# Kernel tuning notes

Hardware: AMD Instinct MI355X
Metric: run time of the kernel (lower is better)

## Reference

```python
import jax, jax.numpy as jnp
import numpy as np
import math

D_MODEL = 96
D_STATE = 16
D_CONV = 3
EXPAND = 2
D_INNER = EXPAND * D_MODEL          # 192
DT_RANK = math.ceil(D_MODEL / 16)   # 6
B_SZ, H_SZ, W_SZ = 2, 56, 56


def setup_inputs() -> dict:
    key = jax.random.key(0)
    ks = jax.random.split(key, 10)
    x = jax.random.normal(ks[0], (B_SZ, H_SZ, W_SZ, D_MODEL), jnp.float32)
    W_in = jax.random.normal(ks[1], (D_MODEL, 2 * D_INNER), jnp.float32) * 0.02
    conv_w = jax.random.normal(ks[2], (D_CONV, D_CONV, 1, D_INNER), jnp.float32) * 0.1
    conv_b = jax.random.normal(ks[3], (D_INNER,), jnp.float32) * 0.02
    W_xproj = jax.random.normal(ks[4], (D_INNER, DT_RANK + 2 * D_STATE), jnp.float32) * 0.02
    dt_std = DT_RANK ** -0.5
    W_dt = jax.random.uniform(ks[5], (DT_RANK, D_INNER), jnp.float32, -dt_std, dt_std)
    # dt_proj bias init: inverse-softplus of dt ~ LogUniform(dt_min, dt_max)
    dt_min, dt_max = 1e-3, 1e-1
    dt = jnp.exp(jax.random.uniform(ks[6], (D_INNER,), jnp.float32)
                 * (math.log(dt_max) - math.log(dt_min)) + math.log(dt_min))
    dt = jnp.clip(dt, 1e-4, None)
    b_dt = dt + jnp.log(-jnp.expm1(-dt))
    # A_log initialized to broadcast arange(1..d_state) (as in the source, no log taken)
    A_log = jnp.tile(jnp.arange(1, D_STATE + 1, dtype=jnp.float32)[None, :], (D_INNER, 1))
    D_skip = jnp.ones((D_INNER,), jnp.float32)
    W_out = jax.random.normal(ks[7], (D_INNER, D_MODEL), jnp.float32) * 0.02
    return {"x": x, "W_in": W_in, "conv_w": conv_w, "conv_b": conv_b,
            "W_xproj": W_xproj, "W_dt": W_dt, "b_dt": b_dt,
            "A_log": A_log, "D_skip": D_skip, "W_out": W_out}


def _selective_scan(xs, dt, A, Bm, Cm, D_skip):
    """Canonical Mamba selective scan.
    xs, dt: (G, L, C); Bm, Cm: (G, L, N); A: (C, N); D_skip: (C,).
    h_l = exp(dt_l * A) * h_{l-1} + dt_l * B_l * x_l ;  y_l = <h_l, C_l> + D * x_l
    """
    dA = jnp.exp(dt[..., None] * A)                              # (G,L,C,N)
    dBx = dt[..., None] * Bm[:, :, None, :] * xs[..., None]      # (G,L,C,N)

    def step(h, inp):
        dA_l, dBx_l, C_l = inp                                   # (G,C,N),(G,C,N),(G,N)
        h = dA_l * h + dBx_l
        y = jnp.einsum('gcn,gn->gc', h, C_l)
        return h, y

    G, L, C = xs.shape
    h0 = jnp.zeros((G, C, D_STATE), xs.dtype)
    _, ys = jax.lax.scan(step, h0, (jnp.moveaxis(dA, 1, 0),
                                    jnp.moveaxis(dBx, 1, 0),
                                    jnp.moveaxis(Cm, 1, 0)))
    ys = jnp.moveaxis(ys, 0, 1)                                  # (G,L,C)
    return ys + D_skip * xs


def reference(x, W_in, conv_w, conv_b, W_xproj, W_dt, b_dt, A_log, D_skip, W_out):
    B, H, W, _ = x.shape  # H == W required (source sums transposed scans directly)
    xz = x @ W_in                                                # (B,H,W,2*d_inner)
    xm, z = jnp.split(xz, 2, axis=-1)
    pad = (D_CONV - 1) // 2
    xm = jax.lax.conv_general_dilated(
        xm, conv_w, (1, 1), [(pad, pad), (pad, pad)],
        dimension_numbers=('NHWC', 'HWIO', 'NHWC'),
        feature_group_count=D_INNER) + conv_b                    # depthwise conv
    # 4 scan directions
    xt = jnp.swapaxes(xm, 1, 2)
    xs4 = jnp.stack([xm, jnp.flip(xm, 2), xt, jnp.flip(xt, 1)], 0)  # (4,B,H,W,C)
    G, L = 4 * B, H * W
    xs = xs4.reshape(G, L, D_INNER)
    x_dbl = xs @ W_xproj                                          # (G,L,dt_rank+2N)
    dtr, Bm, Cm = jnp.split(x_dbl, [DT_RANK, DT_RANK + D_STATE], axis=-1)
    dt = jax.nn.softplus(dtr @ W_dt + b_dt)                       # (G,L,d_inner)
    A = -jnp.exp(A_log)                                           # (d_inner, N)
    ys = _selective_scan(xs, dt, A, Bm, Cm, D_skip)               # (G,L,d_inner)
    y = ys.reshape(4, B, H, W, D_INNER).sum(0)                    # sum 4 directions
    y = jax.nn.silu(z) * y
    return y @ W_out                                              # (B,H,W,d_model)
```

## Files before the change

### kernel.cpp

```cpp
#include <hip/hip_runtime.h>
#include <math.h>

#define NPIX 6272
#define LVAL 3136
#define CIN 192
#define NST 16
#define HW 56
#define CHUNK 28
#define NCH 112

__device__ __forceinline__ float softplusf(float v) {
    return (v > 20.0f) ? v : log1pf(expf(v));
}

__device__ __forceinline__ void dir_geom(int d, int b, int& si, int& sj, int& off) {
    if (d == 0)      { si = HW;  sj = 1;   off = b * LVAL; }
    else if (d == 1) { si = HW;  sj = -1;  off = b * LVAL + (HW - 1); }
    else if (d == 2) { si = 1;   sj = HW;  off = b * LVAL; }
    else             { si = -1;  sj = HW;  off = b * LVAL + (HW - 1); }
}

__global__ __launch_bounds__(384) void k_inproj(
    const float* __restrict__ x, const float* __restrict__ W_in,
    float* __restrict__ xm, float* __restrict__ z)
{
    __shared__ __align__(16) float xs[96][20];
    const int p0 = blockIdx.x * 16;
    const int t = threadIdx.x;
    for (int e = t; e < 16 * 96; e += 384) {
        int p = e / 96, kk = e % 96;
        xs[kk][p] = x[p0 * 96 + e];
    }
    __syncthreads();
    float acc[16];
#pragma unroll
    for (int p = 0; p < 16; ++p) acc[p] = 0.f;
    for (int k = 0; k < 96; ++k) {
        float w = W_in[k * 384 + t];
        float4 x0 = *(const float4*)&xs[k][0];
        float4 x1 = *(const float4*)&xs[k][4];
        float4 x2 = *(const float4*)&xs[k][8];
        float4 x3 = *(const float4*)&xs[k][12];
        acc[0]  = fmaf(x0.x, w, acc[0]);  acc[1]  = fmaf(x0.y, w, acc[1]);
        acc[2]  = fmaf(x0.z, w, acc[2]);  acc[3]  = fmaf(x0.w, w, acc[3]);
        acc[4]  = fmaf(x1.x, w, acc[4]);  acc[5]  = fmaf(x1.y, w, acc[5]);
        acc[6]  = fmaf(x1.z, w, acc[6]);  acc[7]  = fmaf(x1.w, w, acc[7]);
        acc[8]  = fmaf(x2.x, w, acc[8]);  acc[9]  = fmaf(x2.y, w, acc[9]);
        acc[10] = fmaf(x2.z, w, acc[10]); acc[11] = fmaf(x2.w, w, acc[11]);
        acc[12] = fmaf(x3.x, w, acc[12]); acc[13] = fmaf(x3.y, w, acc[13]);
        acc[14] = fmaf(x3.z, w, acc[14]); acc[15] = fmaf(x3.w, w, acc[15]);
    }
#pragma unroll
    for (int p = 0; p < 16; ++p) {
        int pix = p0 + p;
        if (t < 192) xm[pix * CIN + t] = acc[p];
        else         z[pix * CIN + (t - 192)] = acc[p];
    }
}

__global__ __launch_bounds__(256) void k_conv(
    const float* __restrict__ xm, const float* __restrict__ cw,
    const float* __restrict__ cb, float* __restrict__ xcv)
{
    int e = blockIdx.x * 256 + threadIdx.x;
    if (e >= NPIX * (CIN / 4)) return;
    int cq = (e % (CIN / 4)) * 4;
    int pix = e / (CIN / 4);
    int w = pix % HW;
    int rest = pix / HW;
    int h = rest % HW;
    int b = rest / HW;
    float4 acc = *(const float4*)&cb[cq];
#pragma unroll
    for (int ky = 0; ky < 3; ++ky) {
        int hh = h + ky - 1;
        if (hh < 0 || hh >= HW) continue;
#pragma unroll
        for (int kx = 0; kx < 3; ++kx) {
            int ww = w + kx - 1;
            if (ww < 0 || ww >= HW) continue;
            float4 xv = *(const float4*)&xm[((b * HW + hh) * HW + ww) * CIN + cq];
            float4 wv = *(const float4*)&cw[(ky * 3 + kx) * CIN + cq];
            acc.x = fmaf(xv.x, wv.x, acc.x);
            acc.y = fmaf(xv.y, wv.y, acc.y);
            acc.z = fmaf(xv.z, wv.z, acc.z);
            acc.w = fmaf(xv.w, wv.w, acc.w);
        }
    }
    *(float4*)&xcv[pix * CIN + cq] = acc;
}

__global__ __launch_bounds__(512) void k_xproj_dt(
    const float* __restrict__ xcv, const float* __restrict__ W_xproj,
    const float* __restrict__ W_dt, const float* __restrict__ b_dt,
    float* __restrict__ Bp, float* __restrict__ Cp, float2* __restrict__ dtx2)
{
    __shared__ __align__(16) float xs[192][28];
    __shared__ float part[2][24][40];
    __shared__ float dtr_lds[24][8];
    const int p0 = blockIdx.x * 24;
    const int t = threadIdx.x;
    for (int e = t; e < 24 * 192; e += 512) {
        int p = e / 192, kk = e % 192;
        int pix = p0 + p;
        xs[kk][p] = (pix < NPIX) ? xcv[pix * CIN + kk] : 0.f;
    }
    __syncthreads();
    const int th = t & 255;
    const int kh = t >> 8;
    const int j  = th % 40;
    const int pq = th / 40;
    if (pq < 6) {
        const int jc = (j < 38) ? j : 37;
        float a0 = 0.f, a1 = 0.f, a2 = 0.f, a3 = 0.f;
        const int k0 = kh * 96;
        for (int k = k0; k < k0 + 96; ++k) {
            float w = W_xproj[k * 38 + jc];
            float4 xv = *(const float4*)&xs[k][pq * 4];
            a0 = fmaf(xv.x, w, a0); a1 = fmaf(xv.y, w, a1);
            a2 = fmaf(xv.z, w, a2); a3 = fmaf(xv.w, w, a3);
        }
        part[kh][pq * 4 + 0][j] = a0;
        part[kh][pq * 4 + 1][j] = a1;
        part[kh][pq * 4 + 2][j] = a2;
        part[kh][pq * 4 + 3][j] = a3;
    }
    __syncthreads();
    if (kh == 0 && pq < 6 && j < 38) {
#pragma unroll
        for (int q = 0; q < 4; ++q) {
            int p = pq * 4 + q;
            float r = part[0][p][j] + part[1][p][j];
            int pix = p0 + p;
            if (j < 6) dtr_lds[p][j] = r;
            if (pix < NPIX) {
                if (j < 6)       ;
                else if (j < 22) Bp[pix * NST + (j - 6)] = r;
                else             Cp[pix * NST + (j - 22)] = r;
            }
        }
    }
    __syncthreads();
    for (int e = t; e < 24 * 192; e += 512) {
        int p = e / 192, c = e % 192;
        int pix = p0 + p;
        if (pix >= NPIX) continue;
        float v = b_dt[c];
#pragma unroll
        for (int r = 0; r < 6; ++r)
            v = fmaf(dtr_lds[p][r], W_dt[r * CIN + c], v);
        dtx2[(size_t)pix * CIN + c] = make_float2(softplusf(v), xs[c][p]);
    }
}

__global__ __launch_bounds__(384) void k_scan_p1(
    const float2* __restrict__ dtx2, const float* __restrict__ Bp,
    const float* __restrict__ A_log,
    float* __restrict__ Sd, float* __restrict__ qbuf)
{
    constexpr int CPR = HW / CHUNK;
    __shared__ __align__(16) float Bs[CHUNK * NST];
    const int g = blockIdx.y;
    const int k = blockIdx.x;
    const int ch = blockIdx.z;
    const int t = threadIdx.x;
    const int wv = t >> 6;
    const int lane = t & 63;
    const int cl = lane & 15, nh = lane >> 4;
    const int c = ch * 96 + wv * 16 + cl;
    const int n0 = nh * 4;
    const int d = g >> 1, b = g & 1;
    int si, sj, off;
    dir_geom(d, b, si, sj, off);
    const int base = off + (k / CPR) * si + ((k % CPR) * CHUNK) * sj;

    for (int e = t; e < CHUNK * NST; e += 384) {
        int jj = e >> 4, n = e & 15;
        Bs[e] = Bp[(base + jj * sj) * NST + n];
    }

    const float LOG2E = 1.4426950408889634f;
    float a2[4];
    {
        float4 v = *(const float4*)(A_log + c * NST + n0);
        a2[0] = -expf(v.x) * LOG2E;
        a2[1] = -expf(v.y) * LOG2E;
        a2[2] = -expf(v.z) * LOG2E;
        a2[3] = -expf(v.w) * LOG2E;
    }
    __syncthreads();

    float h[4];
#pragma unroll
    for (int i = 0; i < 4; ++i) h[i] = 0.f;
    float Sdt = 0.f;

    const float2* dp = dtx2 + (size_t)base * CIN + c;
    const ptrdiff_t dstep = (ptrdiff_t)sj * CIN;

#define P1_STEP(DVV, JJ) do {                                            \
        float dt_c = (DVV).x, x_c = (DVV).y;                             \
        float dtx = dt_c * x_c;                                          \
        Sdt += dt_c;                                                     \
        float4 t0 = *(const float4*)(Bs + (JJ) * NST + n0);              \
        float Bv[4] = {t0.x, t0.y, t0.z, t0.w};                          \
        _Pragma("unroll")                                                \
        for (int i = 0; i < 4; ++i) {                                    \
            float dA = exp2f(dt_c * a2[i]);                              \
            h[i] = fmaf(dA, h[i], dtx * Bv[i]);                          \
        }                                                                \
    } while (0)

    float2 v0 = dp[0];
    float2 v1 = dp[dstep];
    float2 v2 = dp[2 * dstep];
    float2 v3 = dp[3 * dstep];
    for (int jj = 0; jj < CHUNK; jj += 4) {
        const int j4 = (jj + 4 < CHUNK) ? jj + 4 : CHUNK - 4;
        float2 nv0 = dp[(ptrdiff_t)(j4 + 0) * dstep];
        float2 nv1 = dp[(ptrdiff_t)(j4 + 1) * dstep];
        float2 nv2 = dp[(ptrdiff_t)(j4 + 2) * dstep];
        float2 nv3 = dp[(ptrdiff_t)(j4 + 3) * dstep];
        P1_STEP(v0, jj + 0);
        P1_STEP(v1, jj + 1);
        P1_STEP(v2, jj + 2);
        P1_STEP(v3, jj + 3);
        v0 = nv0; v1 = nv1; v2 = nv2; v3 = nv3;
    }
#undef P1_STEP

    if (nh == 0)
        Sd[(size_t)(k * 8 + g) * CIN + c] = Sdt;
    float4* qd = (float4*)(qbuf + ((size_t)(k * 8 + g) * CIN + c) * NST + n0);
    qd[0] = make_float4(h[0], h[1], h[2], h[3]);
}

__global__ __launch_bounds__(256) void k_scan_fix(
    const float* __restrict__ Sd, const float* __restrict__ A_log,
    float* __restrict__ qbuf, int nch)
{
    const int g = blockIdx.y;
    const int lo = blockIdx.x * 256 + threadIdx.x;
    const int c = lo >> 4;
    const float LOG2E = 1.4426950408889634f;
    const float a2t = -expf(A_log[lo]) * LOG2E;
    const size_t stride = (size_t)8 * CIN * NST;
    const size_t sstride = (size_t)8 * CIN;
    size_t idx  = (size_t)g * CIN * NST + lo;
    size_t pidx = idx;
    size_t sidx = (size_t)g * CIN + c;
    float Sv[8], qr[8];
#pragma unroll
    for (int i = 0; i < 8; ++i) {
        Sv[i] = Sd[sidx]; qr[i] = qbuf[pidx];
        sidx += sstride; pidx += stride;
    }
    float h = 0.f;
    for (int k = 0; k < nch; k += 8) {
        float Sn[8], qn[8];
        if (k + 8 < nch) {
#pragma unroll
            for (int i = 0; i < 8; ++i) {
                Sn[i] = Sd[sidx + (size_t)i * sstride];
                qn[i] = qbuf[pidx + (size_t)i * stride];
            }
        } else {
#pragma unroll
            for (int i = 0; i < 8; ++i) { Sn[i] = 0.f; qn[i] = 0.f; }
        }
#pragma unroll
        for (int i = 0; i < 8; ++i) {
            qbuf[idx] = h;
            float P = exp2f(a2t * Sv[i]);
            h = fmaf(P, h, qr[i]);
            idx += stride;
        }
#pragma unroll
        for (int i = 0; i < 8; ++i) { Sv[i] = Sn[i]; qr[i] = qn[i]; }
        sidx += (size_t)8 * sstride;
        pidx += (size_t)8 * stride;
    }
}

__global__ __launch_bounds__(384) void k_scan_p2(
    const float2* __restrict__ dtx2, const float* __restrict__ Bp,
    const float* __restrict__ Cp, const float* __restrict__ A_log,
    const float* __restrict__ D_skip,
    const float* __restrict__ qbuf, float* __restrict__ Y4)
{
    constexpr int CPR = HW / CHUNK;
    __shared__ __align__(16) float Bs[CHUNK * NST];
    __shared__ __align__(16) float Cs[CHUNK * NST];
    const int g = blockIdx.y;
    const int k = blockIdx.x;
    const int ch = blockIdx.z;
    const int t = threadIdx.x;
    const int wv = t >> 6;
    const int lane = t & 63;
    const int cl = lane & 15, nh = lane >> 4;
    const int c = ch * 96 + wv * 16 + cl;
    const int n0 = nh * 4;
    const int d = g >> 1, b = g & 1;
    int si, sj, off;
    dir_geom(d, b, si, sj, off);
    const int base = off + (k / CPR) * si + ((k % CPR) * CHUNK) * sj;

    for (int e = t; e < CHUNK * NST; e += 384) {
        int jj = e >> 4, n = e & 15;
        int pa = (base + jj * sj) * NST + n;
        Bs[e] = Bp[pa];
        Cs[e] = Cp[pa];
    }

    const float LOG2E = 1.4426950408889634f;
    float a2[4];
    {
        float4 v = *(const float4*)(A_log + c * NST + n0);
        a2[0] = -expf(v.x) * LOG2E;
        a2[1] = -expf(v.y) * LOG2E;
        a2[2] = -expf(v.z) * LOG2E;
        a2[3] = -expf(v.w) * LOG2E;
    }
    const float Dc = D_skip[c];

    float h[4];
    {
        float4 v0q = *(const float4*)(qbuf + ((size_t)(k * 8 + g) * CIN + c) * NST + n0);
        h[0]=v0q.x; h[1]=v0q.y; h[2]=v0q.z; h[3]=v0q.w;
    }
    __syncthreads();

    float* yo = Y4 + ((size_t)d * NPIX + (size_t)b * LVAL + (size_t)k * CHUNK) * CIN;

    const float2* dp = dtx2 + (size_t)base * CIN + c;
    const ptrdiff_t dstep = (ptrdiff_t)sj * CIN;

#define P2_STEP(DVV, JJ) do {                                            \
        float dt_c = (DVV).x, x_c = (DVV).y;                             \
        float dtx = dt_c * x_c;                                          \
        float4 t0 = *(const float4*)(Bs + (JJ) * NST + n0);              \
        float4 u0 = *(const float4*)(Cs + (JJ) * NST + n0);              \
        float Bv[4] = {t0.x, t0.y, t0.z, t0.w};                          \
        float Cv[4] = {u0.x, u0.y, u0.z, u0.w};                          \
        float yc0 = 0.f, yc1 = 0.f;                                      \
        _Pragma("unroll")                                                \
        for (int i = 0; i < 4; i += 2) {                                 \
            float dA0 = exp2f(dt_c * a2[i]);                             \
            float dA1 = exp2f(dt_c * a2[i+1]);                           \
            h[i]   = fmaf(dA0, h[i],   dtx * Bv[i]);                     \
            h[i+1] = fmaf(dA1, h[i+1], dtx * Bv[i+1]);                   \
            yc0 = fmaf(h[i],   Cv[i],   yc0);                            \
            yc1 = fmaf(h[i+1], Cv[i+1], yc1);                            \
        }                                                                \
        float yc = yc0 + yc1;                                            \
        yc += __shfl_xor(yc, 16, 64);                                    \
        yc += __shfl_xor(yc, 32, 64);                                    \
        if (nh == 0)                                                     \
            yo[(JJ) * CIN + c] = fmaf(Dc, x_c, yc);                      \
    } while (0)

    float2 v0 = dp[0];
    float2 v1 = dp[dstep];
    float2 v2 = dp[2 * dstep];
    float2 v3 = dp[3 * dstep];
    for (int jj = 0; jj < CHUNK; jj += 4) {
        const int j4 = (jj + 4 < CHUNK) ? jj + 4 : CHUNK - 4;
        float2 nv0 = dp[(ptrdiff_t)(j4 + 0) * dstep];
        float2 nv1 = dp[(ptrdiff_t)(j4 + 1) * dstep];
        float2 nv2 = dp[(ptrdiff_t)(j4 + 2) * dstep];
        float2 nv3 = dp[(ptrdiff_t)(j4 + 3) * dstep];
        P2_STEP(v0, jj + 0);
        P2_STEP(v1, jj + 1);
        P2_STEP(v2, jj + 2);
        P2_STEP(v3, jj + 3);
        v0 = nv0; v1 = nv1; v2 = nv2; v3 = nv3;
    }
#undef P2_STEP
}

__global__ __launch_bounds__(384) void k_gateout(
    const float* __restrict__ Y4, const float* __restrict__ z,
    const float* __restrict__ W_out, float* __restrict__ out)
{
    __shared__ __align__(16) float xs[192][20];
    const int p0 = blockIdx.x * 16;
    const int t = threadIdx.x;
    const size_t NP = (size_t)NPIX * CIN;
    for (int e = t; e < 16 * 192; e += 384) {
        int p = e / 192, c = e % 192;
        size_t idx = (size_t)(p0 + p) * CIN + c;
        float s = Y4[idx] + Y4[idx + NP] + Y4[idx + 2 * NP] + Y4[idx + 3 * NP];
        float zz = z[idx];
        float sig = 1.f / (1.f + expf(-zz));
        xs[c][p] = zz * sig * s;
    }
    __syncthreads();
    const int j  = t % 96;
    const int ph = t / 96;
    float acc[4] = {0.f, 0.f, 0.f, 0.f};
    for (int k = 0; k < 192; ++k) {
        float w = W_out[k * 96 + j];
        float4 xv = *(const float4*)&xs[k][ph * 4];
        acc[0] = fmaf(xv.x, w, acc[0]); acc[1] = fmaf(xv.y, w, acc[1]);
        acc[2] = fmaf(xv.z, w, acc[2]); acc[3] = fmaf(xv.w, w, acc[3]);
    }
#pragma unroll
    for (int p = 0; p < 4; ++p)
        out[(p0 + ph * 4 + p) * 96 + j] = acc[p];
}

extern "C" void kernel_launch(void* const* d_in, const int* in_sizes, int n_in,
                              void* d_out, int out_size, void* d_ws, size_t ws_size,
                              hipStream_t stream) {
    const float* x      = (const float*)d_in[0];
    const float* W_in   = (const float*)d_in[1];
    const float* conv_w = (const float*)d_in[2];
    const float* conv_b = (const float*)d_in[3];
    const float* W_xproj= (const float*)d_in[4];
    const float* W_dt   = (const float*)d_in[5];
    const float* b_dt   = (const float*)d_in[6];
    const float* A_log  = (const float*)d_in[7];
    const float* D_skip = (const float*)d_in[8];
    const float* W_out  = (const float*)d_in[9];
    float* out = (float*)d_out;

    float* ws   = (float*)d_ws;
    float* xm   = ws;
    float* z    = xm  + NPIX * CIN;
    float* xcv  = z   + NPIX * CIN;
    float2* dtx2= (float2*)(xcv + NPIX * CIN);
    float* Bp   = (float*)(dtx2 + (size_t)NPIX * CIN);
    float* Cp   = Bp  + NPIX * NST;
    float* Y4   = Cp  + NPIX * NST;
    float* Sd   = Y4  + (size_t)4 * NPIX * CIN;
    float* qbuf = Sd  + (size_t)NCH * 8 * CIN;

    k_inproj  <<<NPIX / 16, 384, 0, stream>>>(x, W_in, xm, z);
    k_conv    <<<(NPIX * (CIN / 4)) / 256, 256, 0, stream>>>(xm, conv_w, conv_b, xcv);
    k_xproj_dt<<<(NPIX + 23) / 24, 512, 0, stream>>>(xcv, W_xproj, W_dt, b_dt, Bp, Cp, dtx2);
    k_scan_p1 <<<dim3(NCH, 8, 2), 384, 0, stream>>>(dtx2, Bp, A_log, Sd, qbuf);
    k_scan_fix<<<dim3(12, 8), 256, 0, stream>>>(Sd, A_log, qbuf, NCH);
    k_scan_p2 <<<dim3(NCH, 8, 2), 384, 0, stream>>>(dtx2, Bp, Cp, A_log, D_skip, qbuf, Y4);
    k_gateout <<<NPIX / 16, 384, 0, stream>>>(Y4, z, W_out, out);
}
```

Measured before the change: 194.1 us.

## Pair scan directions per block sharing LDS-staged dt/x/B/C chunks

Scan kernels now process two directions per block: row blocks run forward and reversed sweeps over the same chunk, column blocks exploit that directions 2 and 3 share the same chunk scan and only differ in carried state. dt/x pairs are staged into shared memory once per chunk instead of being loaded strided from global per step. This halves input traffic and grid size, trading fewer blocks and longer per-block serial loops for less redundant memory access.

Result: slower. 258.8 us (+33.3%).

```diff
diff --git a/kernel.cpp b/kernel.cpp
--- a/kernel.cpp
+++ b/kernel.cpp
@@ -11,13 +11,6 @@
 
 __device__ __forceinline__ float softplusf(float v) {
     return (v > 20.0f) ? v : log1pf(expf(v));
-}
-
-__device__ __forceinline__ void dir_geom(int d, int b, int& si, int& sj, int& off) {
-    if (d == 0)      { si = HW;  sj = 1;   off = b * LVAL; }
-    else if (d == 1) { si = HW;  sj = -1;  off = b * LVAL + (HW - 1); }
-    else if (d == 2) { si = 1;   sj = HW;  off = b * LVAL; }
-    else             { si = -1;  sj = HW;  off = b * LVAL + (HW - 1); }
 }
 
 __global__ __launch_bounds__(384) void k_inproj(
@@ -158,25 +151,29 @@
     const float* __restrict__ A_log,
     float* __restrict__ Sd, float* __restrict__ qbuf)
 {
-    constexpr int CPR = HW / CHUNK;
     __shared__ __align__(16) float Bs[CHUNK * NST];
-    const int g = blockIdx.y;
+    __shared__ __align__(16) float2 dts[CHUNK][96];
     const int k = blockIdx.x;
+    const int pr = blockIdx.y >> 1, b = blockIdx.y & 1;
     const int ch = blockIdx.z;
     const int t = threadIdx.x;
-    const int wv = t >> 6;
-    const int lane = t & 63;
+    const int wv = t >> 6, lane = t & 63;
     const int cl = lane & 15, nh = lane >> 4;
     const int c = ch * 96 + wv * 16 + cl;
+    const int cloc = wv * 16 + cl;
     const int n0 = nh * 4;
-    const int d = g >> 1, b = g & 1;
-    int si, sj, off;
-    dir_geom(d, b, si, sj, off);
-    const int base = off + (k / CPR) * si + ((k % CPR) * CHUNK) * sj;
+    const int i2 = k >> 1, jh = k & 1;
+    const int pbase = (pr == 0) ? (b * LVAL + i2 * HW + jh * 28)
+                                : (b * LVAL + (jh * 28) * HW + i2);
+    const int pstep = (pr == 0) ? 1 : HW;
 
     for (int e = t; e < CHUNK * NST; e += 384) {
         int jj = e >> 4, n = e & 15;
-        Bs[e] = Bp[(base + jj * sj) * NST + n];
+        Bs[e] = Bp[(pbase + jj * pstep) * NST + n];
+    }
+    for (int e = t; e < CHUNK * 96; e += 384) {
+        int jj = e / 96, cc = e % 96;
+        dts[jj][cc] = dtx2[(size_t)(pbase + jj * pstep) * CIN + ch * 96 + cc];
     }
 
     const float LOG2E = 1.4426950408889634f;
@@ -190,49 +187,49 @@
     }
     __syncthreads();
 
-    float h[4];
-#pragma unroll
-    for (int i = 0; i < 4; ++i) h[i] = 0.f;
-    float Sdt = 0.f;
-
-    const float2* dp = dtx2 + (size_t)base * CIN + c;
-    const ptrdiff_t dstep = (ptrdiff_t)sj * CIN;
-
-#define P1_STEP(DVV, JJ) do {                                            \
-        float dt_c = (DVV).x, x_c = (DVV).y;                             \
+#define P1_STEP(JJ, H, SACC) do {                                        \
+        float2 dv = dts[(JJ)][cloc];                                     \
+        float dt_c = dv.x, x_c = dv.y;                                   \
         float dtx = dt_c * x_c;                                          \
-        Sdt += dt_c;                                                     \
+        SACC += dt_c;                                                    \
         float4 t0 = *(const float4*)(Bs + (JJ) * NST + n0);              \
         float Bv[4] = {t0.x, t0.y, t0.z, t0.w};                          \
         _Pragma("unroll")                                                \
         for (int i = 0; i < 4; ++i) {                                    \
             float dA = exp2f(dt_c * a2[i]);                              \
-            h[i] = fmaf(dA, h[i], dtx * Bv[i]);                          \
+            H[i] = fmaf(dA, H[i], dtx * Bv[i]);                          \
         }                                                                \
+        (void)x_c;                                                       \
     } while (0)
 
-    float2 v0 = dp[0];
-    float2 v1 = dp[dstep];
-    float2 v2 = dp[2 * dstep];
-    float2 v3 = dp[3 * dstep];
-    for (int jj = 0; jj < CHUNK; jj += 4) {
-        const int j4 = (jj + 4 < CHUNK) ? jj + 4 : CHUNK - 4;
-        float2 nv0 = dp[(ptrdiff_t)(j4 + 0) * dstep];
-        float2 nv1 = dp[(ptrdiff_t)(j4 + 1) * dstep];
-        float2 nv2 = dp[(ptrdiff_t)(j4 + 2) * dstep];
-        float2 nv3 = dp[(ptrdiff_t)(j4 + 3) * dstep];
-        P1_STEP(v0, jj + 0);
-        P1_STEP(v1, jj + 1);
-        P1_STEP(v2, jj + 2);
-        P1_STEP(v3, jj + 3);
-        v0 = nv0; v1 = nv1; v2 = nv2; v3 = nv3;
+#define P1_WRITE(KK, G, H, SACC) do {                                    \
+        if (nh == 0)                                                     \
+            Sd[(size_t)((KK) * 8 + (G)) * CIN + c] = (SACC);             \
+        float4* qd = (float4*)(qbuf +                                    \
+            ((size_t)((KK) * 8 + (G)) * CIN + c) * NST + n0);            \
+        qd[0] = make_float4(H[0], H[1], H[2], H[3]);                     \
+    } while (0)
+
+    if (pr == 0) {
+        float h[4] = {0.f, 0.f, 0.f, 0.f};
+        float Sdt = 0.f;
+        for (int jj = 0; jj < CHUNK; ++jj) P1_STEP(jj, h, Sdt);
+        P1_WRITE(k, b, h, Sdt);
+        float hb[4] = {0.f, 0.f, 0.f, 0.f};
+        float Sb = 0.f;
+        for (int s = 0; s < CHUNK; ++s) { int jj = 27 - s; P1_STEP(jj, hb, Sb); }
+        const int k1 = i2 * 2 + (1 - jh);
+        P1_WRITE(k1, 2 + b, hb, Sb);
+    } else {
+        float h[4] = {0.f, 0.f, 0.f, 0.f};
+        float Sdt = 0.f;
+        for (int jj = 0; jj < CHUNK; ++jj) P1_STEP(jj, h, Sdt);
+        P1_WRITE(k, 4 + b, h, Sdt);
+        const int k3 = (55 - i2) * 2 + jh;
+        P1_WRITE(k3, 6 + b, h, Sdt);
     }
 #undef P1_STEP
-
-    if (nh == 0)
-        Sd[(size_t)(k * 8 + g) * CIN + c] = Sdt;
-    float4* qd = (float4*)(qbuf + ((size_t)(k * 8 + g) * CIN + c) * NST + n0);
-    qd[0] = make_float4(h[0], h[1], h[2], h[3]);
+#undef P1_WRITE
 }
 
 __global__ __launch_bounds__(256) void k_scan_fix(
@@ -288,28 +285,32 @@
     const float* __restrict__ D_skip,
     const float* __restrict__ qbuf, float* __restrict__ Y4)
 {
-    constexpr int CPR = HW / CHUNK;
     __shared__ __align__(16) float Bs[CHUNK * NST];
     __shared__ __align__(16) float Cs[CHUNK * NST];
-    const int g = blockIdx.y;
+    __shared__ __align__(16) float2 dts[CHUNK][96];
     const int k = blockIdx.x;
+    const int pr = blockIdx.y >> 1, b = blockIdx.y & 1;
     const int ch = blockIdx.z;
     const int t = threadIdx.x;
-    const int wv = t >> 6;
-    const int lane = t & 63;
+    const int wv = t >> 6, lane = t & 63;
     const int cl = lane & 15, nh = lane >> 4;
     const int c = ch * 96 + wv * 16 + cl;
+    const int cloc = wv * 16 + cl;
     const int n0 = nh * 4;
-    const int d = g >> 1, b = g & 1;
-    int si, sj, off;
-    dir_geom(d, b, si, sj, off);
-    const int base = off + (k / CPR) * si + ((k % CPR) * CHUNK) * sj;
+    const int i2 = k >> 1, jh = k & 1;
+    const int pbase = (pr == 0) ? (b * LVAL + i2 * HW + jh * 28)
+                                : (b * LVAL + (jh * 28) * HW + i2);
+    const int pstep = (pr == 0) ? 1 : HW;
 
     for (int e = t; e < CHUNK * NST; e += 384) {
         int jj = e >> 4, n = e & 15;
-        int pa = (base + jj * sj) * NST + n;
+        int pa = (pbase + jj * pstep) * NST + n;
         Bs[e] = Bp[pa];
         Cs[e] = Cp[pa];
+    }
+    for (int e = t; e < CHUNK * 96; e += 384) {
+        int jj = e / 96, cc = e % 96;
+        dts[jj][cc] = dtx2[(size_t)(pbase + jj * pstep) * CIN + ch * 96 + cc];
     }
 
     const float LOG2E = 1.4426950408889634f;
@@ -322,21 +323,17 @@
         a2[3] = -expf(v.w) * LOG2E;
     }
     const float Dc = D_skip[c];
-
-    float h[4];
-    {
-        float4 v0q = *(const float4*)(qbuf + ((size_t)(k * 8 + g) * CIN + c) * NST + n0);
-        h[0]=v0q.x; h[1]=v0q.y; h[2]=v0q.z; h[3]=v0q.w;
-    }
-    __syncthreads();
-
-    float* yo = Y4 + ((size_t)d * NPIX + (size_t)b * LVAL + (size_t)k * CHUNK) * CIN;
-
-    const float2* dp = dtx2 + (size_t)base * CIN + c;
-    const ptrdiff_t dstep = (ptrdiff_t)sj * CIN;
-
-#define P2_STEP(DVV, JJ) do {                                            \
-        float dt_c = (DVV).x, x_c = (DVV).y;                             \
+    __syncthreads();
+
+#define LOAD_H(H, KK, G) do {                                            \
+        float4 vq = *(const float4*)(qbuf +                              \
+            ((size_t)((KK) * 8 + (G)) * CIN + c) * NST + n0);            \
+        H[0] = vq.x; H[1] = vq.y; H[2] = vq.z; H[3] = vq.w;              \
+    } while (0)
+
+#define P2_STEP(JJ, H, YO, POS) do {                                     \
+        float2 dv = dts[(JJ)][cloc];                                     \
+        float dt_c = dv.x, x_c = dv.y;                                   \
         float dtx = dt_c * x_c;                                          \
         float4 t0 = *(const float4*)(Bs + (JJ) * NST + n0);              \
         float4 u0 = *(const float4*)(Cs + (JJ) * NST + n0);              \
@@ -347,35 +344,72 @@
         for (int i = 0; i < 4; i += 2) {                                 \
             float dA0 = exp2f(dt_c * a2[i]);                             \
             float dA1 = exp2f(dt_c * a2[i+1]);                           \
-            h[i]   = fmaf(dA0, h[i],   dtx * Bv[i]);                     \
-            h[i+1] = fmaf(dA1, h[i+1], dtx * Bv[i+1]);                   \
-            yc0 = fmaf(h[i],   Cv[i],   yc0);                            \
-            yc1 = fmaf(h[i+1], Cv[i+1], yc1);                            \
+            H[i]   = fmaf(dA0, H[i],   dtx * Bv[i]);                     \
+            H[i+1] = fmaf(dA1, H[i+1], dtx * Bv[i+1]);                   \
+            yc0 = fmaf(H[i],   Cv[i],   yc0);                            \
+            yc1 = fmaf(H[i+1], Cv[i+1], yc1);                            \
         }                                                                \
         float yc = yc0 + yc1;                                            \
         yc += __shfl_xor(yc, 16, 64);                                    \
         yc += __shfl_xor(yc, 32, 64);                                    \
         if (nh == 0)                                                     \
-            yo[(JJ) * CIN + c] = fmaf(Dc, x_c, yc);                      \
+            (YO)[(POS) * CIN + c] = fmaf(Dc, x_c, yc);                   \
     } while (0)
 
-    float2 v0 = dp[0];
-    float2 v1 = dp[dstep];
-    float2 v2 = dp[2 * dstep];
-    float2 v3 = dp[3 * dstep];
-    for (int jj = 0; jj < CHUNK; jj += 4) {
-        const int j4 = (jj + 4 < CHUNK) ? jj + 4 : CHUNK - 4;
-        float2 nv0 = dp[(ptrdiff_t)(j4 + 0) * dstep];
-        float2 nv1 = dp[(ptrdiff_t)(j4 + 1) * dstep];
-        float2 nv2 = dp[(ptrdiff_t)(j4 + 2) * dstep];
-        float2 nv3 = dp[(ptrdiff_t)(j4 + 3) * dstep];
-        P2_STEP(v0, jj + 0);
-        P2_STEP(v1, jj + 1);
-        P2_STEP(v2, jj + 2);
-        P2_STEP(v3, jj + 3);
-        v0 = nv0; v1 = nv1; v2 = nv2; v3 = nv3;
+    if (pr == 0) {
+        float h[4];
+        LOAD_H(h, k, b);
+        float* yo0 = Y4 + ((size_t)0 * NPIX + (size_t)b * LVAL + (size_t)k * CHUNK) * CIN;
+        for (int jj = 0; jj < CHUNK; ++jj) P2_STEP(jj, h, yo0, jj);
+        const int k1 = i2 * 2 + (1 - jh);
+        float h1[4];
+        LOAD_H(h1, k1, 2 + b);
+        float* yo1 = Y4 + ((size_t)1 * NPIX + (size_t)b * LVAL + (size_t)k1 * CHUNK) * CIN;
+        for (int s = 0; s < CHUNK; ++s) { int jj = 27 - s; P2_STEP(jj, h1, yo1, s); }
+    } else {
+        const int k3 = (55 - i2) * 2 + jh;
+        float h2[4], h3[4];
+        LOAD_H(h2, k, 4 + b);
+        LOAD_H(h3, k3, 6 + b);
+        float* yo2 = Y4 + ((size_t)2 * NPIX + (size_t)b * LVAL + (size_t)k * CHUNK) * CIN;
+        float* yo3 = Y4 + ((size_t)3 * NPIX + (size_t)b * LVAL + (size_t)k3 * CHUNK) * CIN;
+        for (int jj = 0; jj < CHUNK; ++jj) {
+            float2 dv = dts[jj][cloc];
+            float dt_c = dv.x, x_c = dv.y;
+            float dtx = dt_c * x_c;
+            float4 t0 = *(const float4*)(Bs + jj * NST + n0);
+            float4 u0 = *(const float4*)(Cs + jj * NST + n0);
+            float Bv[4] = {t0.x, t0.y, t0.z, t0.w};
+            float Cv[4] = {u0.x, u0.y, u0.z, u0.w};
+            float y2a = 0.f, y2b = 0.f, y3a = 0.f, y3b = 0.f;
+#pragma unroll
+            for (int i = 0; i < 4; i += 2) {
+                float dA0 = exp2f(dt_c * a2[i]);
+                float dA1 = exp2f(dt_c * a2[i+1]);
+                float dB0 = dtx * Bv[i], dB1 = dtx * Bv[i+1];
+                h2[i]   = fmaf(dA0, h2[i],   dB0);
+                h2[i+1] = fmaf(dA1, h2[i+1], dB1);
+                h3[i]   = fmaf(dA0, h3[i],   dB0);
+                h3[i+1] = fmaf(dA1, h3[i+1], dB1);
+                y2a = fmaf(h2[i],   Cv[i],   y2a);
+                y2b = fmaf(h2[i+1], Cv[i+1], y2b);
+                y3a = fmaf(h3[i],   Cv[i],   y3a);
+                y3b = fmaf(h3[i+1], Cv[i+1], y3b);
+            }
+            float y2 = y2a + y2b;
+            float y3 = y3a + y3b;
+            y2 += __shfl_xor(y2, 16, 64);
+            y2 += __shfl_xor(y2, 32, 64);
+            y3 += __shfl_xor(y3, 16, 64);
+            y3 += __shfl_xor(y3, 32, 64);
+            if (nh == 0) {
+                yo2[jj * CIN + c] = fmaf(Dc, x_c, y2);
+                yo3[jj * CIN + c] = fmaf(Dc, x_c, y3);
+            }
+        }
     }
 #undef P2_STEP
+#undef LOAD_H
 }
 
 __global__ __launch_bounds__(384) void k_gateout(
@@ -438,8 +472,8 @@
     k_inproj  <<<NPIX / 16, 384, 0, stream>>>(x, W_in, xm, z);
     k_conv    <<<(NPIX * (CIN / 4)) / 256, 256, 0, stream>>>(xm, conv_w, conv_b, xcv);
     k_xproj_dt<<<(NPIX + 23) / 24, 512, 0, stream>>>(xcv, W_xproj, W_dt, b_dt, Bp, Cp, dtx2);
-    k_scan_p1 <<<dim3(NCH, 8, 2), 384, 0, stream>>>(dtx2, Bp, A_log, Sd, qbuf);
+    k_scan_p1 <<<dim3(NCH, 4, 2), 384, 0, stream>>>(dtx2, Bp, A_log, Sd, qbuf);
     k_scan_fix<<<dim3(12, 8), 256, 0, stream>>>(Sd, A_log, qbuf, NCH);
-    k_scan_p2 <<<dim3(NCH, 8, 2), 384, 0, stream>>>(dtx2, Bp, Cp, A_log, D_skip, qbuf, Y4);
+    k_scan_p2 <<<dim3(NCH, 4, 2), 384, 0, stream>>>(dtx2, Bp, Cp, A_log, D_skip, qbuf, Y4);
     k_gateout <<<NPIX / 16, 384, 0, stream>>>(Y4, z, W_out, out);
 }
```
